# Kernel tuning notes

Hardware: AMD Instinct MI355X
Metric: run time of the kernel (lower is better)

Reference implementation:

```python
import jax, jax.numpy as jnp
import numpy as np

B, S, D = 2, 2048, 4096
H, KVH, DH = 32, 8, 128
KVD = KVH * DH  # 1024
EPS = 1e-6
SCALING = DH ** -0.5


def _rms_norm(x, scale):
    xf = x.astype(jnp.float32)
    var = jnp.mean(xf * xf, axis=-1, keepdims=True)
    return (xf * jax.lax.rsqrt(var + EPS)).astype(x.dtype) * scale


def _rotate_half(x):
    half = x.shape[-1] // 2
    return jnp.concatenate([-x[..., half:], x[..., :half]], axis=-1)


def setup_inputs() -> dict:
    key = jax.random.key(0)
    ks = jax.random.split(key, 5)
    hidden_states = jax.random.normal(ks[0], (B, S, D), dtype=jnp.float32)
    w_qkv = jax.random.normal(ks[1], (D, D + 2 * KVD), dtype=jnp.float32) * 0.02
    w_out = jax.random.normal(ks[2], (D, D), dtype=jnp.float32) * 0.02
    q_scale = jnp.ones((D,), dtype=jnp.float32)
    k_scale = jnp.ones((KVD,), dtype=jnp.float32)
    # real rotary tables: cos/sin of positions, broadcast to batch
    inv_freq = 1.0 / (10000.0 ** (np.arange(0, DH, 2, dtype=np.float32) / DH))
    pos = np.arange(S, dtype=np.float32)
    freqs = np.outer(pos, inv_freq)            # [S, DH/2]
    emb = np.concatenate([freqs, freqs], -1)   # [S, DH]
    cos_cached = jnp.broadcast_to(jnp.asarray(np.cos(emb)), (B, S, DH))
    sin_cached = jnp.broadcast_to(jnp.asarray(np.sin(emb)), (B, S, DH))
    # causal mask: True = masked
    idx = jnp.arange(S)
    attention_mask = (idx[None, :] > idx[:, None])[None, None].repeat(B, 0)  # [B,1,S,S] bool
    return {
        "hidden_states": hidden_states, "w_qkv": w_qkv, "w_out": w_out,
        "q_scale": q_scale, "k_scale": k_scale,
        "cos_cached": cos_cached, "sin_cached": sin_cached,
        "attention_mask": attention_mask,
    }


def reference(hidden_states, w_qkv, w_out, q_scale, k_scale, cos_cached, sin_cached, attention_mask):
    b, s, _ = hidden_states.shape
    qkv = jnp.einsum("bsd,de->bse", hidden_states, w_qkv)
    q, k, v = jnp.split(qkv, [D, D + KVD], axis=-1)
    # qk-norm applied pre-view over full projected dim (non-qwen3 path)
    q = _rms_norm(q, q_scale)
    k = _rms_norm(k, k_scale)
    q = q.reshape(b, s, H, DH).transpose(0, 2, 1, 3)    # [B,H,S,DH]
    k = k.reshape(b, s, KVH, DH).transpose(0, 2, 1, 3)  # [B,KVH,S,DH]
    v = v.reshape(b, s, KVH, DH).transpose(0, 2, 1, 3)
    cos = cos_cached[:, None]  # [B,1,S,DH]
    sin = sin_cached[:, None]
    q = q * cos + _rotate_half(q) * sin
    k = k * cos + _rotate_half(k) * sin
    # repeat KV heads to match query heads (GQA)
    n_rep = H // KVH
    k = jnp.repeat(k, n_rep, axis=1)
    v = jnp.repeat(v, n_rep, axis=1)
    scores = jnp.einsum("bhsd,bhtd->bhst", q, k) * SCALING
    scores = jnp.where(attention_mask, jnp.float32(-10000.0), scores)
    attn = jax.nn.softmax(scores.astype(jnp.float32), axis=-1).astype(q.dtype)
    out = jnp.einsum("bhst,bhtd->bhsd", attn, v)
    out = out.transpose(0, 2, 1, 3).reshape(b, s, H * DH)
    return jnp.einsum("bsd,de->bse", out, w_out)
```

## Files before the change

### kernel.cpp

```cpp
#include <hip/hip_runtime.h>
#include <hip/hip_bf16.h>
#include <cstdint>
#include <cstddef>

#define BB 2
#define SS 2048
#define DD 4096
#define HH 32
#define KVH 8
#define DH 128
#define KVD 1024
#define SCALE 0.08838834764831845f
#define QSC 0.1275178745225f

typedef __attribute__((ext_vector_type(8))) short short8;
typedef __attribute__((ext_vector_type(4))) float f32x4;

typedef __attribute__((address_space(1))) void GV;
typedef __attribute__((address_space(3))) void LV;

__device__ __forceinline__ void async16(const void* g, void* l) {
  __builtin_amdgcn_global_load_lds((GV*)g, (LV*)l, 16, 0, 0);
}

__device__ __forceinline__ unsigned short f2bf(float x) {
  union { float f; uint32_t u; } v; v.f = x;
  uint32_t r = (v.u + 0x7fffu + ((v.u >> 16) & 1u)) >> 16;
  return (unsigned short)r;
}
__device__ __forceinline__ float bf2f(unsigned short b) {
  union { uint32_t u; float f; } v; v.u = ((uint32_t)b) << 16; return v.f;
}
__device__ __forceinline__ f32x4 mfma16(short8 a, short8 b, f32x4 c) {
  return __builtin_amdgcn_mfma_f32_16x16x32_bf16(a, b, c, 0, 0, 0);
}

__global__ __launch_bounds__(256) void cast_bf16_kernel(
    const float* __restrict__ in, unsigned short* __restrict__ out, int n4) {
  int i = blockIdx.x * 256 + threadIdx.x;
  if (i >= n4) return;
  float4 v = ((const float4*)in)[i];
  ushort4 o;
  o.x = f2bf(v.x); o.y = f2bf(v.y); o.z = f2bf(v.z); o.w = f2bf(v.w);
  ((ushort4*)out)[i] = o;
}

__global__ __launch_bounds__(256) void transpose_cast_kernel(
    const float* __restrict__ in, unsigned short* __restrict__ out, int R, int C) {
  __shared__ unsigned short tile[32][33];
  const int tx = threadIdx.x, ty = threadIdx.y;
  const int c0 = blockIdx.x * 32, r0 = blockIdx.y * 32;
  for (int i = ty; i < 32; i += 8)
    tile[i][tx] = f2bf(in[(size_t)(r0 + i) * C + c0 + tx]);
  __syncthreads();
  for (int i = ty; i < 32; i += 8)
    out[(size_t)(c0 + i) * R + r0 + tx] = tile[tx][i];
}

template <typename OutT>
__global__ __launch_bounds__(256, 2) void gemm_bt(
    const unsigned short* __restrict__ A, const unsigned short* __restrict__ Bt,
    OutT* __restrict__ C, int M, int N, int K) {
  __shared__ __align__(16) unsigned short As[4096];
  __shared__ __align__(16) unsigned short Bs[4096];
  const int tid = threadIdx.x;
  const int wave = tid >> 6, lane = tid & 63, quad = lane >> 4, l16 = lane & 15;
  const int m0 = blockIdx.x * 128, n0 = blockIdx.y * 128;
  const int wm = (wave & 1) * 64, wn = (wave >> 1) * 64;
  f32x4 acc[4][4] = {};
  const int sr = tid >> 2, sc = (tid & 3) * 8;
  const unsigned short* Ag = A + (size_t)(m0 + sr) * K + sc;
  const unsigned short* Bg = Bt + (size_t)(n0 + sr) * K + sc;
  unsigned short* AsW = As + wave * 512;
  unsigned short* BsW = Bs + wave * 512;
  for (int k0 = 0; k0 < K; k0 += 32) {
    __syncthreads();
    async16(Ag + k0, AsW);
    async16(Ag + (size_t)64 * K + k0, AsW + 2048);
    async16(Bg + k0, BsW);
    async16(Bg + (size_t)64 * K + k0, BsW + 2048);
    __syncthreads();
    short8 af[4], bf[4];
#pragma unroll
    for (int i = 0; i < 4; i++) {
      af[i] = *(const short8*)&As[(wm + i * 16 + l16) * 32 + quad * 8];
      bf[i] = *(const short8*)&Bs[(wn + i * 16 + l16) * 32 + quad * 8];
    }
#pragma unroll
    for (int mi = 0; mi < 4; mi++)
#pragma unroll
      for (int ni = 0; ni < 4; ni++)
        acc[mi][ni] = mfma16(af[mi], bf[ni], acc[mi][ni]);
  }
#pragma unroll
  for (int mi = 0; mi < 4; mi++)
#pragma unroll
    for (int ni = 0; ni < 4; ni++)
#pragma unroll
      for (int r = 0; r < 4; r++) {
        int row = m0 + wm + mi * 16 + quad * 4 + r;
        int col = n0 + wn + ni * 16 + l16;
        float v = acc[mi][ni][r];
        if constexpr (sizeof(OutT) == 4) C[(size_t)row * N + col] = v;
        else                             C[(size_t)row * N + col] = (OutT)f2bf(v);
      }
}

__global__ __launch_bounds__(256) void rmsnorm_rope_kernel(
    const unsigned short* __restrict__ qkv,
    const float* __restrict__ q_scale, const float* __restrict__ k_scale,
    const float* __restrict__ cosc, const float* __restrict__ sinc,
    unsigned short* __restrict__ qo,
    unsigned short* __restrict__ ko,
    unsigned short* __restrict__ vo)
{
  const int row = blockIdx.x;
  const int b = row >> 11, s = row & 2047;
  const int tid = threadIdx.x;
  const unsigned short* qr = qkv + (size_t)row * 6144;
  float sq = 0.f, sk = 0.f;
  for (int c = tid; c < 4096; c += 256) { float v = bf2f(qr[c]); sq += v * v; }
  for (int c = tid; c < 1024; c += 256) { float v = bf2f(qr[4096 + c]); sk += v * v; }
#pragma unroll
  for (int off = 32; off; off >>= 1) {
    sq += __shfl_down(sq, off, 64);
    sk += __shfl_down(sk, off, 64);
  }
  __shared__ float redq[4], redk[4];
  if ((tid & 63) == 0) { redq[tid >> 6] = sq; redk[tid >> 6] = sk; }
  __syncthreads();
  sq = redq[0] + redq[1] + redq[2] + redq[3];
  sk = redk[0] + redk[1] + redk[2] + redk[3];
  const float rq = rsqrtf(sq * (1.f / 4096.f) + 1e-6f);
  const float rk = rsqrtf(sk * (1.f / 1024.f) + 1e-6f);
  const float* cp = cosc + (size_t)row * 128;
  const float* sp = sinc + (size_t)row * 128;
  for (int c = tid; c < 4096; c += 256) {
    int d = c & 127, hh = c >> 7;
    float v = bf2f(qr[c]) * rq * q_scale[c];
    int c2 = (d < 64) ? c + 64 : c - 64;
    float v2 = bf2f(qr[c2]) * rq * q_scale[c2];
    float rot = (d < 64) ? -v2 : v2;
    qo[((size_t)(b * HH + hh) * SS + s) * DH + d] = f2bf((v * cp[d] + rot * sp[d]) * QSC);
  }
  for (int c = tid; c < 1024; c += 256) {
    int d = c & 127, hh = c >> 7;
    float v = bf2f(qr[4096 + c]) * rk * k_scale[c];
    int kc2 = (d < 64) ? c + 64 : c - 64;
    float v2 = bf2f(qr[4096 + kc2]) * rk * k_scale[kc2];
    float rot = (d < 64) ? -v2 : v2;
    ko[((size_t)(b * KVH + hh) * SS + s) * DH + d] = f2bf(v * cp[d] + rot * sp[d]);
  }
  for (int c = tid; c < 1024; c += 256) {
    int d = c & 127, hh = c >> 7;
    vo[((size_t)(b * KVH + hh) * DH + d) * SS + s] = qr[5120 + c];
  }
}

__global__ __launch_bounds__(256, 2) void flash_attn(
    const unsigned short* __restrict__ Q,
    const unsigned short* __restrict__ Kr,
    const unsigned short* __restrict__ Vt,
    unsigned short* __restrict__ O)
{
  __shared__ __align__(16) unsigned short Ks[8192];
  __shared__ __align__(16) unsigned short Vs[8192];
  __shared__ __align__(16) unsigned int   Ps[4][1024];
  const int tid = threadIdx.x, wave = tid >> 6, lane = tid & 63;
  const int quad = lane >> 4, l16 = lane & 15;
  const int bh = blockIdx.x, b = bh >> 5, h = bh & 31;
  const int kvh = h >> 2;
  const int qbase = ((int)gridDim.y - 1 - (int)blockIdx.y) * 128;
  const unsigned short* Qb = Q + (size_t)(b * HH + h) * SS * DH;
  short8 qf[2][4];
#pragma unroll
  for (int mi = 0; mi < 2; mi++) {
    const unsigned short* Qp = Qb + (size_t)(qbase + mi * 64 + wave * 16 + l16) * DH + quad * 8;
#pragma unroll
    for (int c = 0; c < 4; c++) qf[mi][c] = *(const short8*)(Qp + c * 32);
  }
  const unsigned short* Kg = Kr + (size_t)(b * KVH + kvh) * SS * DH;
  const unsigned short* Vg = Vt + (size_t)(b * KVH + kvh) * DH * SS;
  int bK[4], bV[4];
#pragma unroll
  for (int j = 0; j < 4; j++) {
    const int kk = wave * 16 + j * 4 + quad;
    const int gd = l16 ^ ((j * 4 + quad) & 15);
    bK[j] = kk * 128 + gd * 8;
    const int dd = (wave * 4 + j) * 8 + (lane >> 3);
    const int gk = (lane & 7) ^ ((lane >> 3) & 7);
    bV[j] = dd * 2048 + gk * 8;
  }
  f32x4 o[2][8] = {};
  float m_i[2] = {-1e30f, -1e30f}, l_i[2] = {0.f, 0.f};
  const int ndiag = qbase >> 6;
  const int nkt = ndiag + 2;
  for (int kt = 0; kt < nkt; kt++) {
    const int k0 = kt * 64;
    __syncthreads();
#pragma unroll
    for (int j = 0; j < 4; j++) {
      async16(Kg + (size_t)k0 * 128 + bK[j], Ks + (wave * 4 + j) * 512);
      async16(Vg + k0 + bV[j], Vs + (wave * 4 + j) * 512);
    }
    __syncthreads();
    f32x4 st[4][2] = {};
#pragma unroll
    for (int km = 0; km < 4; km++) {
      const unsigned short* krow = Ks + (km * 16 + l16) * 128;
#pragma unroll
      for (int c = 0; c < 4; c++) {
        short8 kf = *(const short8*)(krow + (((c * 4 + quad) ^ l16) * 8));
        st[km][0] = mfma16(kf, qf[0][c], st[km][0]);
        st[km][1] = mfma16(kf, qf[1][c], st[km][1]);
      }
    }
    const bool mtile = (kt >= ndiag);
    float alpha[2];
#pragma unroll
    for (int mi = 0; mi < 2; mi++) {
      if (mtile) {
        const int qg = qbase + mi * 64 + wave * 16 + l16;
#pragma unroll
        for (int km = 0; km < 4; km++)
#pragma unroll
          for (int r = 0; r < 4; r++)
            if (k0 + km * 16 + quad * 4 + r > qg) st[km][mi][r] = -1e4f;
      }
      float tmax = -3e38f;
#pragma unroll
      for (int km = 0; km < 4; km++)
#pragma unroll
        for (int r = 0; r < 4; r++) tmax = fmaxf(tmax, st[km][mi][r]);
      tmax = fmaxf(tmax, __shfl_xor(tmax, 16, 64));
      tmax = fmaxf(tmax, __shfl_xor(tmax, 32, 64));
      const float mn = fmaxf(m_i[mi], tmax);
      alpha[mi] = __builtin_amdgcn_exp2f(m_i[mi] - mn);
      m_i[mi] = mn;
      float rs = 0.f;
#pragma unroll
      for (int km = 0; km < 4; km++)
#pragma unroll
        for (int r = 0; r < 4; r++) {
          float e = __builtin_amdgcn_exp2f(st[km][mi][r] - mn);
          st[km][mi][r] = e;
          rs += e;
        }
      rs += __shfl_xor(rs, 16, 64);
      rs += __shfl_xor(rs, 32, 64);
      l_i[mi] = l_i[mi] * alpha[mi] + rs;
      unsigned int* pw = &Ps[wave][(mi * 16 + l16) * 32 + (quad & 1) * 2];
#pragma unroll
      for (int km = 0; km < 4; km++) {
        const int g = (km * 2 + (quad >> 1)) ^ (l16 & 7);
        float e0 = st[km][mi][0], e1 = st[km][mi][1], e2 = st[km][mi][2], e3 = st[km][mi][3];
        pw[g * 4]     = __builtin_amdgcn_perm(__builtin_bit_cast(unsigned int, e1),
                                              __builtin_bit_cast(unsigned int, e0), 0x07060302u);
        pw[g * 4 + 1] = __builtin_amdgcn_perm(__builtin_bit_cast(unsigned int, e3),
                                              __builtin_bit_cast(unsigned int, e2), 0x07060302u);
      }
    }
    if (__any((alpha[0] != 1.f) || (alpha[1] != 1.f))) {
#pragma unroll
      for (int mi = 0; mi < 2; mi++) {
        float ar[4];
#pragma unroll
        for (int r = 0; r < 4; r++)
          ar[r] = __shfl(alpha[mi], (lane & 48) + quad * 4 + r, 64);
#pragma unroll
        for (int f = 0; f < 8; f++)
#pragma unroll
          for (int r = 0; r < 4; r++) o[mi][f][r] *= ar[r];
      }
    }
#pragma unroll
    for (int kc = 0; kc < 2; kc++) {
      short8 pa[2];
#pragma unroll
      for (int mi = 0; mi < 2; mi++) {
        const int g = (kc * 4 + quad) ^ (l16 & 7);
        uint4 pv4 = *(const uint4*)&Ps[wave][(mi * 16 + l16) * 32 + g * 4];
        pa[mi] = __builtin_bit_cast(short8, pv4);
      }
#pragma unroll
      for (int f = 0; f < 8; f++) {
        const int d = f * 16 + l16;
        short8 vf = *(const short8*)(Vs + d * 64 + (((kc * 4 + quad) ^ (l16 & 7)) * 8));
        o[0][f] = mfma16(pa[0], vf, o[0][f]);
        o[1][f] = mfma16(pa[1], vf, o[1][f]);
      }
    }
  }
  float il[2][4];
#pragma unroll
  for (int mi = 0; mi < 2; mi++)
#pragma unroll
    for (int r = 0; r < 4; r++) {
      float lv = __shfl(l_i[mi], (lane & 48) + quad * 4 + r, 64);
      il[mi][r] = 1.f / lv;
    }
#pragma unroll
  for (int mi = 0; mi < 2; mi++) {
    unsigned short* Op = O + (size_t)(b * SS + qbase + mi * 64 + wave * 16 + quad * 4) * DD + h * DH + l16;
#pragma unroll
    for (int f = 0; f < 8; f++)
#pragma unroll
      for (int r = 0; r < 4; r++)
        Op[(size_t)r * DD + f * 16] = f2bf(o[mi][f][r] * il[mi][r]);
  }
}

extern "C" void kernel_launch(void* const* d_in, const int* in_sizes, int n_in,
                              void* d_out, int out_size, void* d_ws, size_t ws_size,
                              hipStream_t stream) {
  const float* hs      = (const float*)d_in[0];
  const float* wqkv    = (const float*)d_in[1];
  const float* wout    = (const float*)d_in[2];
  const float* q_scale = (const float*)d_in[3];
  const float* k_scale = (const float*)d_in[4];
  const float* cosc    = (const float*)d_in[5];
  const float* sinc    = (const float*)d_in[6];
  float* out = (float*)d_out;

  unsigned short* ws = (unsigned short*)d_ws;
  unsigned short* wqkvT = ws;
  unsigned short* woutT = wqkvT + 25165824;
  unsigned short* hsb   = woutT + 16777216;
  unsigned short* qkv   = hsb + 16777216;
  unsigned short* qrope = wqkvT;
  unsigned short* krope = wqkvT + 16777216;
  unsigned short* vT    = wqkvT + 16777216 + 4194304;
  unsigned short* attno = hsb;

  cast_bf16_kernel<<<16384, 256, 0, stream>>>(hs, hsb, 4194304);
  transpose_cast_kernel<<<dim3(192, 128), dim3(32, 8), 0, stream>>>(wqkv, wqkvT, 4096, 6144);
  transpose_cast_kernel<<<dim3(128, 128), dim3(32, 8), 0, stream>>>(wout, woutT, 4096, 4096);
  gemm_bt<unsigned short><<<dim3(32, 48), 256, 0, stream>>>(hsb, wqkvT, qkv, 4096, 6144, 4096);
  rmsnorm_rope_kernel<<<4096, 256, 0, stream>>>(qkv, q_scale, k_scale, cosc, sinc,
                                                qrope, krope, vT);
  flash_attn<<<dim3(64, 16), 256, 0, stream>>>(qrope, krope, vT, attno);
  gemm_bt<float><<<dim3(32, 32), 256, 0, stream>>>(attno, woutT, out, 4096, 4096, 4096);
}
```

Baseline: 837.2 us.

## Swizzle GEMM LDS layout, vectorize rmsnorm-rope, split V transpose into tiled kernel

Applies an XOR swizzle to the GEMM's LDS staging so that the 16-byte fragment reads avoid LDS bank conflicts. Rewrites the rmsnorm/rope kernel to use vectorized 16-byte loads and stores, keeping the row in registers for both the norm and the rotation. Moves the V transpose into its own shared-memory tiled kernel so the old strided scattered stores become coalesced writes. This adds one kernel launch and relies on the swizzle being consistent between the async writes and the fragment reads.

Measured after the change: 799.6 us. 1.05x faster.

```diff
diff --git a/kernel.cpp b/kernel.cpp
--- a/kernel.cpp
+++ b/kernel.cpp
@@ -55,6 +55,21 @@
   __syncthreads();
   for (int i = ty; i < 32; i += 8)
     out[(size_t)(c0 + i) * R + r0 + tx] = tile[tx][i];
+}
+
+__global__ __launch_bounds__(256) void transpose_v_kernel(
+    const unsigned short* __restrict__ qkv, unsigned short* __restrict__ vo) {
+  __shared__ unsigned short tile[32][33];
+  const int s0 = blockIdx.x * 32, d0 = blockIdx.y * 32;
+  const int b = blockIdx.z >> 3, kvh = blockIdx.z & 7;
+  const int tx = threadIdx.x, ty = threadIdx.y;
+  const unsigned short* ip = qkv + 5120 + (size_t)kvh * 128 + d0 + tx;
+  for (int i = ty; i < 32; i += 8)
+    tile[i][tx] = ip[(size_t)(b * SS + s0 + i) * 6144];
+  __syncthreads();
+  unsigned short* op = vo + (size_t)(b * KVH + kvh) * DH * SS + s0 + tx;
+  for (int i = ty; i < 32; i += 8)
+    op[(size_t)(d0 + i) * SS] = tile[tx][i];
 }
 
 template <typename OutT>
@@ -68,11 +83,13 @@
   const int m0 = blockIdx.x * 128, n0 = blockIdx.y * 128;
   const int wm = (wave & 1) * 64, wn = (wave >> 1) * 64;
   f32x4 acc[4][4] = {};
-  const int sr = tid >> 2, sc = (tid & 3) * 8;
-  const unsigned short* Ag = A + (size_t)(m0 + sr) * K + sc;
-  const unsigned short* Bg = Bt + (size_t)(n0 + sr) * K + sc;
+  const int sr = tid >> 2;
+  const int sg = (tid & 3) ^ ((tid >> 3) & 3);
+  const unsigned short* Ag = A + (size_t)(m0 + sr) * K + sg * 8;
+  const unsigned short* Bg = Bt + (size_t)(n0 + sr) * K + sg * 8;
   unsigned short* AsW = As + wave * 512;
   unsigned short* BsW = Bs + wave * 512;
+  const int pg = (quad ^ ((l16 >> 1) & 3)) * 8;
   for (int k0 = 0; k0 < K; k0 += 32) {
     __syncthreads();
     async16(Ag + k0, AsW);
@@ -83,8 +100,8 @@
     short8 af[4], bf[4];
 #pragma unroll
     for (int i = 0; i < 4; i++) {
-      af[i] = *(const short8*)&As[(wm + i * 16 + l16) * 32 + quad * 8];
-      bf[i] = *(const short8*)&Bs[(wn + i * 16 + l16) * 32 + quad * 8];
+      af[i] = *(const short8*)&As[(wm + i * 16 + l16) * 32 + pg];
+      bf[i] = *(const short8*)&Bs[(wn + i * 16 + l16) * 32 + pg];
     }
 #pragma unroll
     for (int mi = 0; mi < 4; mi++)
@@ -111,16 +128,26 @@
     const float* __restrict__ q_scale, const float* __restrict__ k_scale,
     const float* __restrict__ cosc, const float* __restrict__ sinc,
     unsigned short* __restrict__ qo,
-    unsigned short* __restrict__ ko,
-    unsigned short* __restrict__ vo)
+    unsigned short* __restrict__ ko)
 {
   const int row = blockIdx.x;
   const int b = row >> 11, s = row & 2047;
   const int tid = threadIdx.x;
   const unsigned short* qr = qkv + (size_t)row * 6144;
+  short8 qv0 = *(const short8*)&qr[tid * 8];
+  short8 qv1 = *(const short8*)&qr[2048 + tid * 8];
+  ushort4 kv = *(const ushort4*)&qr[4096 + tid * 4];
   float sq = 0.f, sk = 0.f;
-  for (int c = tid; c < 4096; c += 256) { float v = bf2f(qr[c]); sq += v * v; }
-  for (int c = tid; c < 1024; c += 256) { float v = bf2f(qr[4096 + c]); sk += v * v; }
+#pragma unroll
+  for (int e = 0; e < 8; e++) {
+    float a = bf2f((unsigned short)qv0[e]); sq += a * a;
+    float c = bf2f((unsigned short)qv1[e]); sq += c * c;
+  }
+  float kf[4];
+#pragma unroll
+  for (int e = 0; e < 4; e++) {
+    kf[e] = bf2f(((const unsigned short*)&kv)[e]); sk += kf[e] * kf[e];
+  }
 #pragma unroll
   for (int off = 32; off; off >>= 1) {
     sq += __shfl_down(sq, off, 64);
@@ -135,25 +162,35 @@
   const float rk = rsqrtf(sk * (1.f / 1024.f) + 1e-6f);
   const float* cp = cosc + (size_t)row * 128;
   const float* sp = sinc + (size_t)row * 128;
-  for (int c = tid; c < 4096; c += 256) {
-    int d = c & 127, hh = c >> 7;
-    float v = bf2f(qr[c]) * rq * q_scale[c];
-    int c2 = (d < 64) ? c + 64 : c - 64;
-    float v2 = bf2f(qr[c2]) * rq * q_scale[c2];
-    float rot = (d < 64) ? -v2 : v2;
-    qo[((size_t)(b * HH + hh) * SS + s) * DH + d] = f2bf((v * cp[d] + rot * sp[d]) * QSC);
-  }
-  for (int c = tid; c < 1024; c += 256) {
-    int d = c & 127, hh = c >> 7;
-    float v = bf2f(qr[4096 + c]) * rk * k_scale[c];
-    int kc2 = (d < 64) ? c + 64 : c - 64;
-    float v2 = bf2f(qr[4096 + kc2]) * rk * k_scale[kc2];
-    float rot = (d < 64) ? -v2 : v2;
-    ko[((size_t)(b * KVH + hh) * SS + s) * DH + d] = f2bf(v * cp[d] + rot * sp[d]);
-  }
-  for (int c = tid; c < 1024; c += 256) {
-    int d = c & 127, hh = c >> 7;
-    vo[((size_t)(b * KVH + hh) * DH + d) * SS + s] = qr[5120 + c];
+#pragma unroll
+  for (int it = 0; it < 2; it++) {
+    const int c = it * 2048 + tid * 8;
+    const int d = c & 127, hh = c >> 7;
+    short8 v8 = it ? qv1 : qv0;
+    short8 p8 = *(const short8*)&qr[c ^ 64];
+    const float sgn = (d < 64) ? -1.f : 1.f;
+    ushort o8[8];
+#pragma unroll
+    for (int e = 0; e < 8; e++) {
+      float v = bf2f((unsigned short)v8[e]) * rq * q_scale[c + e];
+      float p = bf2f((unsigned short)p8[e]) * rq * q_scale[(c ^ 64) + e];
+      o8[e] = f2bf((v * cp[d + e] + sgn * p * sp[d + e]) * QSC);
+    }
+    *(uint4*)&qo[((size_t)(b * HH + hh) * SS + s) * DH + d] = *(const uint4*)o8;
+  }
+  {
+    const int c = tid * 4;
+    const int d = c & 127, hh = c >> 7;
+    ushort4 p4 = *(const ushort4*)&qr[4096 + (c ^ 64)];
+    const float sgn = (d < 64) ? -1.f : 1.f;
+    ushort o4[4];
+#pragma unroll
+    for (int e = 0; e < 4; e++) {
+      float v = kf[e] * rk * k_scale[c + e];
+      float p = bf2f(((const unsigned short*)&p4)[e]) * rk * k_scale[(c ^ 64) + e];
+      o4[e] = f2bf(v * cp[d + e] + sgn * p * sp[d + e]);
+    }
+    *(uint2*)&ko[((size_t)(b * KVH + hh) * SS + s) * DH + d] = *(const uint2*)o4;
   }
 }
 
@@ -337,7 +374,8 @@
   transpose_cast_kernel<<<dim3(128, 128), dim3(32, 8), 0, stream>>>(wout, woutT, 4096, 4096);
   gemm_bt<unsigned short><<<dim3(32, 48), 256, 0, stream>>>(hsb, wqkvT, qkv, 4096, 6144, 4096);
   rmsnorm_rope_kernel<<<4096, 256, 0, stream>>>(qkv, q_scale, k_scale, cosc, sinc,
-                                                qrope, krope, vT);
+                                                qrope, krope);
+  transpose_v_kernel<<<dim3(64, 4, 16), dim3(32, 8), 0, stream>>>(qkv, vT);
   flash_attn<<<dim3(64, 16), 256, 0, stream>>>(qrope, krope, vT, attno);
   gemm_bt<float><<<dim3(32, 32), 256, 0, stream>>>(attno, woutT, out, 4096, 4096, 4096);
 }
```
